# Optimization experiments

Hardware: AMD Instinct MI355X
Metric: run time of the kernel (lower is better)

The kernel has to match this reference:

```python
import jax, jax.numpy as jnp
from jax import lax
import numpy as np

N, E = 10000, 120000
IN_DIM = 128
HID = 32        # hidden_dim
HEADS = 8
OUT = 32        # out_dim
HD = HID * HEADS  # 256
EPS = 1e-5


def _bn(x, g, b):
    # BatchNorm1d (training-mode batch stats, deterministic reference)
    mu = x.mean(0)
    var = x.var(0)
    return g * (x - mu) * lax.rsqrt(var + EPS) + b


def _seg_softmax(logits, seg, n):
    # softmax over edges grouped by destination node, per head
    m = jax.ops.segment_max(logits, seg, num_segments=n)
    ex = jnp.exp(logits - m[seg])
    s = jax.ops.segment_sum(ex, seg, num_segments=n)
    return ex / (s[seg] + 1e-16)


def _gat_layer(h, src, dst, fc_w, a_l, a_r, bn_g, bn_b, heads, out, residual):
    n = h.shape[0]
    h_in = h
    feat = (h @ fc_w).reshape(n, heads, out)      # [N,H,D]
    el = (feat * a_l).sum(-1)                     # [N,H]
    er = (feat * a_r).sum(-1)
    logits = jax.nn.leaky_relu(el[src] + er[dst], 0.2)  # [E,H]
    alpha = _seg_softmax(logits, dst, n)
    rst = jax.ops.segment_sum(alpha[..., None] * feat[src], dst, num_segments=n)
    rst = rst.reshape(n, heads * out)
    rst = _bn(rst, bn_g, bn_b)
    rst = jax.nn.elu(rst)
    if residual:
        rst = h_in + rst
    return rst


def setup_inputs():
    key = jax.random.key(0)
    ks = jax.random.split(key, 20)
    s = 0.02
    d = {}
    d["h"] = jax.random.normal(ks[0], (N, IN_DIM), jnp.float32)
    d["e"] = jax.random.normal(ks[1], (E, IN_DIM), jnp.float32)
    d["src"] = jax.random.randint(ks[2], (E,), 0, N, jnp.int32)
    d["dst"] = jax.random.randint(ks[3], (E,), 0, N, jnp.int32)
    d["W_emb"] = jax.random.normal(ks[4], (IN_DIM, HD)) * s
    d["b_emb"] = jnp.zeros((HD,))
    d["W_p1"] = jax.random.normal(ks[5], (IN_DIM, HID * HID)) * s
    d["b_p1"] = jnp.zeros((HID * HID,))
    d["W_p2"] = jax.random.normal(ks[6], (IN_DIM, HID)) * s
    d["b_p2"] = jnp.zeros((HID,))
    d["W_conv"] = jax.random.normal(ks[7], (1, 2, 3)) * s  # Conv1d(2->1,k=3)
    d["b_conv"] = jnp.zeros((1,))
    d["W_ep2"] = jax.random.normal(ks[8], (IN_DIM, HD)) * s
    d["b_ep2"] = jnp.zeros((HD,))
    d["W_ep3"] = jax.random.normal(ks[9], (HID, HD)) * s
    d["b_ep3"] = jnp.zeros((HD,))
    d["bn_g"] = jnp.ones((HD,))
    d["bn_b"] = jnp.zeros((HD,))
    d["fc1"] = jax.random.normal(ks[10], (HD, HD)) * s
    d["al1"] = jax.random.normal(ks[11], (HEADS, HID)) * s
    d["ar1"] = jax.random.normal(ks[12], (HEADS, HID)) * s
    d["g1"] = jnp.ones((HD,))
    d["b1"] = jnp.zeros((HD,))
    d["fc2"] = jax.random.normal(ks[13], (HD, OUT)) * s
    d["al2"] = jax.random.normal(ks[14], (1, OUT)) * s
    d["ar2"] = jax.random.normal(ks[15], (1, OUT)) * s
    d["g2"] = jnp.ones((OUT,))
    d["b2"] = jnp.zeros((OUT,))
    return d


def reference(h, e, src, dst, W_emb, b_emb, W_p1, b_p1, W_p2, b_p2,
              W_conv, b_conv, W_ep2, b_ep2, W_ep3, b_ep3, bn_g, bn_b,
              fc1, al1, ar1, g1, b1, fc2, al2, ar2, g2, b2):
    # local edge feature: Conv1d over stacked (src,dst) node feats
    edge = jnp.stack([h[src], h[dst]], axis=1)  # [E,2,IN_DIM]
    conv = lax.conv_general_dilated(edge, W_conv, (1,), [(1, 1)],
                                    dimension_numbers=("NCH", "OIH", "NCH"))
    lr_local = conv[:, 0, :] + b_conv[0]         # [E,IN_DIM]
    lr_e_local = lr_local @ W_ep2 + b_ep2        # [E,HD]
    # low-rank global affinity: mm[i,j,k] = sum_d p1[i,k,d]*p2[j,d],
    # gathered only at edges (same math as the dense NxNxHID tensor)
    p1 = (h @ W_p1 + b_p1).reshape(-1, HID, HID)  # [N,HID,HID]
    p2 = h @ W_p2 + b_p2                          # [N,HID]
    lr_glob = jnp.einsum("ekd,ed->ek", p1[src], p2[dst])  # [E,HID]
    lr_e_global = lr_glob @ W_ep3 + b_ep3        # [E,HD]
    e_feat = jax.nn.relu(_bn(lr_e_local + lr_e_global, bn_g, bn_b))
    del e_feat  # default 'dgl' GATLayer ignores e; kept for faithfulness of math
    hh = h @ W_emb + b_emb                       # embedding_h
    hh = _gat_layer(hh, src, dst, fc1, al1, ar1, g1, b1, HEADS, HID, True)
    hh = _gat_layer(hh, src, dst, fc2, al2, ar2, g2, b2, 1, OUT, False)
    return hh
```

## Files before the change

kernel.cpp:

```cpp
#include <hip/hip_runtime.h>
#include <hip/hip_bf16.h>
#include <math.h>


#define HDIM 256
#define NHEADS 8
#define ODIM 32

typedef unsigned short u16;
typedef __attribute__((ext_vector_type(8))) short short8;
typedef __attribute__((ext_vector_type(4))) float f32x4;

__device__ __forceinline__ float bf2f(u16 u) { return __uint_as_float(((unsigned)u) << 16); }
__device__ __forceinline__ u16 f2bf(float f) {
    unsigned x = __float_as_uint(f);
    return (u16)((x + 0x7FFFu + ((x >> 16) & 1u)) >> 16);
}

__global__ __launch_bounds__(256) void prep_kernel(const float* __restrict__ in_h, const float* __restrict__ W_emb,
                                                   const float* __restrict__ fc1, const float* __restrict__ fc2,
                                                   const int* __restrict__ dstv, int* __restrict__ deg,
                                                   u16* __restrict__ Ah, u16* __restrict__ Bemb,
                                                   u16* __restrict__ Bfc1, u16* __restrict__ Bfc2,
                                                   int n4, int E, int N) {
    int job = blockIdx.y;
    int idx = blockIdx.x * 256 + threadIdx.x;
    if (job == 0) {
        if (idx >= n4) return;
        float4 v = ((const float4*)in_h)[idx];
        ushort4 o = {f2bf(v.x), f2bf(v.y), f2bf(v.z), f2bf(v.w)};
        ((ushort4*)Ah)[idx] = o;
        return;
    }
    if (job == 4) {
        if (idx < E) {
            unsigned d = (unsigned)dstv[idx];
            if (d < (unsigned)N) atomicAdd(&deg[d], 1);
        }
        return;
    }
    const float* B;
    u16* O;
    int K, NC;
    if (job == 1) { B = W_emb; O = Bemb; K = 128; NC = 256; }
    else if (job == 2) { B = fc1; O = Bfc1; K = 256; NC = 256; }
    else { B = fc2; O = Bfc2; K = 256; NC = 32; }
    int KB = K / 32;
    int TOT = (NC / 16) * KB * 64;
    if (idx >= TOT) return;
    int lane = idx & 63;
    int kb = (idx >> 6) % KB;
    int ct = (idx >> 6) / KB;
    int n = ct * 16 + (lane & 15);
    int k0 = kb * 32 + (lane >> 4) * 8;
    u16* dst = O + (size_t)idx * 8;
#pragma unroll
    for (int j = 0; j < 8; j++) dst[j] = f2bf(B[(size_t)(k0 + j) * NC + n]);
}

__global__ __launch_bounds__(256) void scan_kernel(const int* __restrict__ deg, int* __restrict__ offs,
                                                   int* __restrict__ cursor, int n) {
    __shared__ int wsum[4];
    int t = threadIdx.x;
    int chunk = (n + 255) / 256;
    int lo = t * chunk, hi = lo + chunk;
    if (hi > n) hi = n;
    if (lo > n) lo = n;
    int s = 0;
    for (int i = lo; i < hi; i++) s += deg[i];
    int v = s;
#pragma unroll
    for (int d = 1; d < 64; d <<= 1) {
        int nb = __shfl_up(v, d, 64);
        if ((t & 63) >= d) v += nb;
    }
    if ((t & 63) == 63) wsum[t >> 6] = v;
    __syncthreads();
    int woff = 0;
#pragma unroll
    for (int w = 0; w < 4; w++)
        if (w < (t >> 6)) woff += wsum[w];
    int run = woff + v - s;
    for (int i = lo; i < hi; i++) {
        offs[i] = run;
        cursor[i] = run;
        run += deg[i];
    }
    if (t == 255) offs[n] = run;
}

__global__ __launch_bounds__(256) void fused_emb_fc1(const u16* __restrict__ Ah, const u16* __restrict__ Bemb,
                                                     const float* __restrict__ bemb, const u16* __restrict__ Bfc1,
                                                     const float* __restrict__ al, const float* __restrict__ ar,
                                                     u16* __restrict__ hh, u16* __restrict__ feat1,
                                                     u16* __restrict__ el, u16* __restrict__ er,
                                                     const int* __restrict__ src, const int* __restrict__ dstv,
                                                     int* __restrict__ cursor, int* __restrict__ srcs,
                                                     int M, int NB, int E, int N) {
    if ((int)blockIdx.x >= NB) {
        int i = ((int)blockIdx.x - NB) * 256 + (int)threadIdx.x;
        if (i < E) {
            unsigned d = (unsigned)dstv[i];
            if (d < (unsigned)N) {
                int p = atomicAdd(&cursor[d], 1);
                if ((unsigned)p < (unsigned)E) srcs[p] = src[i];
            }
        }
        return;
    }
    __shared__ u16 tile[16 * 256];
    const int t = threadIdx.x;
    const int lane = t & 63, w = t >> 6;
    const int rb = (int)blockIdx.x * 16;
    const int m = lane & 15, q = lane >> 4;
    const int arow = rb + m;

    short8 a0[4];
#pragma unroll
    for (int kb = 0; kb < 4; kb++) {
        if (arow < M) a0[kb] = *(const short8*)(Ah + (size_t)arow * 128 + kb * 32 + q * 8);
        else a0[kb] = (short8){0, 0, 0, 0, 0, 0, 0, 0};
    }
    const short8* B8 = (const short8*)Bemb;
#pragma unroll
    for (int ct2 = 0; ct2 < 4; ct2++) {
        const int ct = w * 4 + ct2;
        f32x4 acc = {0.f, 0.f, 0.f, 0.f};
#pragma unroll
        for (int kb = 0; kb < 4; kb++)
            acc = __builtin_amdgcn_mfma_f32_16x16x32_bf16(a0[kb], B8[(ct * 4 + kb) * 64 + lane], acc, 0, 0, 0);
        float bv = bemb[ct * 16 + m];
#pragma unroll
        for (int r = 0; r < 4; r++) {
            int rl = q * 4 + r;
            int ro = rb + rl;
            u16 hv = 0;
            if (ro < M) {
                hv = f2bf(acc[r] + bv);
                hh[(size_t)ro * 256 + ct * 16 + m] = hv;
            }
            int byte = rl * 512 + (ct * 16 + m) * 2;
            tile[(byte ^ ((rl & 7) << 4)) >> 1] = hv;
        }
    }
    __syncthreads();

    short8 af[8];
    {
        int rl = m;
#pragma unroll
        for (int kb = 0; kb < 8; kb++) {
            int byte = rl * 512 + kb * 64 + q * 16;
            af[kb] = *(const short8*)(tile + ((byte ^ ((rl & 7) << 4)) >> 1));
        }
    }
    __syncthreads();

    const short8* Bf = (const short8*)Bfc1;
#pragma unroll
    for (int ct2 = 0; ct2 < 4; ct2++) {
        const int ct = w * 4 + ct2;
        f32x4 acc = {0.f, 0.f, 0.f, 0.f};
#pragma unroll
        for (int kb = 0; kb < 8; kb++)
            acc = __builtin_amdgcn_mfma_f32_16x16x32_bf16(af[kb], Bf[(ct * 8 + kb) * 64 + lane], acc, 0, 0, 0);
#pragma unroll
        for (int r = 0; r < 4; r++) {
            int rl = q * 4 + r;
            int ro = rb + rl;
            u16 v = 0;
            if (ro < M) {
                v = f2bf(acc[r]);
                feat1[(size_t)ro * 256 + ct * 16 + m] = v;
            }
            tile[rl * 256 + ct * 16 + m] = v;
        }
    }
    __syncthreads();

    if (t < 128) {
        int nl = t >> 3, h2 = t & 7;
        int node = rb + nl;
        if (node < M) {
            float a_ = 0.f, b_ = 0.f;
#pragma unroll
            for (int d = 0; d < 32; d++) {
                float fv = bf2f(tile[nl * 256 + h2 * 32 + d]);
                a_ += fv * al[h2 * 32 + d];
                b_ += fv * ar[h2 * 32 + d];
            }
            el[node * 8 + h2] = f2bf(a_);
            er[node * 8 + h2] = f2bf(b_);
        }
    }
}

__device__ __forceinline__ float edgew(float l) {
    l = (l > 0.f) ? l : 0.2f * l;
    l = fminf(fmaxf(l, -30.f), 30.f);
    return __expf(l);
}

__global__ __launch_bounds__(256) void agg1_fused(const u16* __restrict__ feat, const u16* __restrict__ el,
                                                  const u16* __restrict__ er, const int* __restrict__ offs,
                                                  const int* __restrict__ srcs, u16* __restrict__ rst, int N, int E) {
    const int node = blockIdx.x * 4 + (threadIdx.x >> 6);
    const int lane = threadIdx.x & 63;
    if (node >= N) return;
    const int half = lane >> 5;
    const int sl = lane & 31;
    const int h = sl >> 2;
    int beg = offs[node], end = offs[node + 1];
    if (beg < 0) beg = 0;
    if (end > E) end = E;
    int cnt = end - beg;
    if (cnt < 0) cnt = 0;
    float ern = bf2f(er[node * 8 + h]);
    float acc[8] = {0.f, 0.f, 0.f, 0.f, 0.f, 0.f, 0.f, 0.f};
    float sw = 0.f;
    const int myCnt = (cnt - half + 1) >> 1;
    const int jb = beg + half;
    int k = 0;
    int k4 = myCnt & ~3;
    for (; k < k4; k += 4) {
        int j0 = jb + 2 * k;
        int s0 = srcs[j0], s1 = srcs[j0 + 2], s2 = srcs[j0 + 4], s3 = srcs[j0 + 6];
        unsigned c0 = (unsigned)s0 < (unsigned)N, c1 = (unsigned)s1 < (unsigned)N;
        unsigned c2 = (unsigned)s2 < (unsigned)N, c3 = (unsigned)s3 < (unsigned)N;
        s0 = c0 ? s0 : 0; s1 = c1 ? s1 : 0; s2 = c2 ? s2 : 0; s3 = c3 ? s3 : 0;
        u16 e0 = el[s0 * 8 + h], e1 = el[s1 * 8 + h], e2 = el[s2 * 8 + h], e3 = el[s3 * 8 + h];
        short8 f0 = *(const short8*)(feat + (size_t)s0 * 256 + sl * 8);
        short8 f1 = *(const short8*)(feat + (size_t)s1 * 256 + sl * 8);
        short8 f2 = *(const short8*)(feat + (size_t)s2 * 256 + sl * 8);
        short8 f3 = *(const short8*)(feat + (size_t)s3 * 256 + sl * 8);
        float w0 = c0 ? edgew(bf2f(e0) + ern) : 0.f;
        float w1 = c1 ? edgew(bf2f(e1) + ern) : 0.f;
        float w2 = c2 ? edgew(bf2f(e2) + ern) : 0.f;
        float w3 = c3 ? edgew(bf2f(e3) + ern) : 0.f;
        sw += w0 + w1 + w2 + w3;
#pragma unroll
        for (int q = 0; q < 8; q++)
            acc[q] += w0 * bf2f((u16)f0[q]) + w1 * bf2f((u16)f1[q]) + w2 * bf2f((u16)f2[q]) + w3 * bf2f((u16)f3[q]);
    }
    for (; k < myCnt; k++) {
        int j = jb + 2 * k;
        int s = srcs[j];
        if ((unsigned)s >= (unsigned)N) continue;
        float wv = edgew(bf2f(el[s * 8 + h]) + ern);
        short8 fv = *(const short8*)(feat + (size_t)s * 256 + sl * 8);
        sw += wv;
#pragma unroll
        for (int q = 0; q < 8; q++) acc[q] += wv * bf2f((u16)fv[q]);
    }
#pragma unroll
    for (int q = 0; q < 8; q++) acc[q] += __shfl_xor(acc[q], 32, 64);
    sw += __shfl_xor(sw, 32, 64);
    if (half == 0) {
        float inv = 1.f / (sw + 1e-16f);
        short8 o;
#pragma unroll
        for (int q = 0; q < 8; q++) o[q] = (short)f2bf(acc[q] * inv);
        *(short8*)(rst + (size_t)node * 256 + sl * 8) = o;
    }
}

__global__ __launch_bounds__(256) void bn_stats256(const u16* __restrict__ X, float* __restrict__ stats,
                                                   int rows, int RPB) {
    __shared__ float ps[256][8], ps2[256][8];
    int t = threadIdx.x;
    int rg = t >> 5, cg = t & 31;
    int rbeg = blockIdx.x * RPB;
    int rend = rbeg + RPB;
    if (rend > rows) rend = rows;
    float s[8] = {0.f, 0.f, 0.f, 0.f, 0.f, 0.f, 0.f, 0.f};
    float s2[8] = {0.f, 0.f, 0.f, 0.f, 0.f, 0.f, 0.f, 0.f};
    for (int r = rbeg + rg; r < rend; r += 8) {
        short8 v = *(const short8*)(X + (size_t)r * 256 + cg * 8);
#pragma unroll
        for (int q = 0; q < 8; q++) {
            float x = bf2f((u16)v[q]);
            s[q] += x;
            s2[q] += x * x;
        }
    }
#pragma unroll
    for (int q = 0; q < 8; q++) { ps[t][q] = s[q]; ps2[t][q] = s2[q]; }
    __syncthreads();
    float a = 0.f, b = 0.f;
#pragma unroll
    for (int g = 0; g < 8; g++) {
        a += ps[g * 32 + (t >> 3)][t & 7];
        b += ps2[g * 32 + (t >> 3)][t & 7];
    }
    atomicAdd(&stats[t], a);
    atomicAdd(&stats[256 + t], b);
}

__global__ __launch_bounds__(256) void bn_stats32(const float* __restrict__ X, float* __restrict__ stats,
                                                  int rows, int RPB) {
    __shared__ float ss[256], ss2[256];
    int t = threadIdx.x, c = t & 31, rs = t >> 5;
    int rbeg = blockIdx.x * RPB;
    int rend = rbeg + RPB;
    if (rend > rows) rend = rows;
    float s = 0.f, s2 = 0.f;
    for (int r = rbeg + rs; r < rend; r += 8) {
        float x = X[(long)r * 32 + c];
        s += x;
        s2 += x * x;
    }
    ss[t] = s;
    ss2[t] = s2;
    __syncthreads();
    if (t < 32) {
        for (int j = 32; j < 256; j += 32) { s += ss[t + j]; s2 += ss2[t + j]; }
        atomicAdd(&stats[c], s);
        atomicAdd(&stats[32 + c], s2);
    }
}

__global__ __launch_bounds__(256) void gemm_fc2_fused(const u16* __restrict__ rst, const u16* __restrict__ hh,
                                                      const float* __restrict__ stats, const float* __restrict__ g,
                                                      const float* __restrict__ b, const u16* __restrict__ Bsw,
                                                      const float* __restrict__ al2, const float* __restrict__ ar2,
                                                      float* __restrict__ feat2, float* __restrict__ el2,
                                                      float* __restrict__ er2, int M, float invN) {
    __shared__ float sc[256], sh[256];
    __shared__ float red[2][256];
    __shared__ float tile[16][32];
    const int t = threadIdx.x;
    {
        float mu = stats[t] * invN;
        float var = fmaxf(stats[256 + t] * invN - mu * mu, 0.f);
        float s = g[t] * rsqrtf(var + 1e-5f);
        sc[t] = s;
        sh[t] = b[t] - mu * s;
    }
    __syncthreads();
    const int lane = t & 63, w = t >> 6;
    const int ct = w & 1, kh = w >> 1;
    const int rb = (int)blockIdx.x * 16;
    const int m = lane & 15, q = lane >> 4;
    const int row = rb + m;
    short8 a[4];
#pragma unroll
    for (int j = 0; j < 4; j++) {
        if (row < M) {
            int k0 = (kh * 4 + j) * 32 + q * 8;
            ushort4 r01 = *(const ushort4*)(rst + (size_t)row * 256 + k0);
            ushort4 r23 = *(const ushort4*)(rst + (size_t)row * 256 + k0 + 4);
            ushort4 h01 = *(const ushort4*)(hh + (size_t)row * 256 + k0);
            ushort4 h23 = *(const ushort4*)(hh + (size_t)row * 256 + k0 + 4);
            u16 rv[8] = {r01.x, r01.y, r01.z, r01.w, r23.x, r23.y, r23.z, r23.w};
            u16 hv[8] = {h01.x, h01.y, h01.z, h01.w, h23.x, h23.y, h23.z, h23.w};
            short8 av;
#pragma unroll
            for (int jj = 0; jj < 8; jj++) {
                int c = k0 + jj;
                float y = sc[c] * bf2f(rv[jj]) + sh[c];
                y = (y > 0.f) ? y : expm1f(y);
                av[jj] = (short)f2bf(bf2f(hv[jj]) + y);
            }
            a[j] = av;
        } else a[j] = (short8){0, 0, 0, 0, 0, 0, 0, 0};
    }
    const short8* B8 = (const short8*)Bsw;
    f32x4 acc = {0.f, 0.f, 0.f, 0.f};
#pragma unroll
    for (int j = 0; j < 4; j++)
        acc = __builtin_amdgcn_mfma_f32_16x16x32_bf16(a[j], B8[(ct * 8 + kh * 4 + j) * 64 + lane], acc, 0, 0, 0);
    if (kh == 1) *(f32x4*)&red[ct][lane * 4] = acc;
    __syncthreads();
    if (kh == 0) {
        f32x4 p = *(const f32x4*)&red[ct][lane * 4];
#pragma unroll
        for (int r = 0; r < 4; r++) {
            int rl = q * 4 + r;
            int ro = rb + rl;
            float v = 0.f;
            if (ro < M) {
                v = acc[r] + p[r];
                feat2[(size_t)ro * 32 + ct * 16 + m] = v;
            }
            tile[rl][ct * 16 + m] = v;
        }
    }
    __syncthreads();
    if (t < 16) {
        int node = rb + t;
        if (node < M) {
            float a_ = 0.f, b_ = 0.f;
#pragma unroll
            for (int d = 0; d < 32; d++) {
                float fv = tile[t][d];
                a_ += fv * al2[d];
                b_ += fv * ar2[d];
            }
            el2[node] = a_;
            er2[node] = b_;
        }
    }
}

__global__ __launch_bounds__(256) void agg2_fused(const float* __restrict__ feat, const float* __restrict__ el,
                                                  const float* __restrict__ er, const int* __restrict__ offs,
                                                  const int* __restrict__ srcs, float* __restrict__ rst,
                                                  int N, int E) {
    const int t = threadIdx.x;
    const int node = blockIdx.x * 8 + (t >> 5);
    const int d = t & 31;
    if (node >= N) return;
    int beg = offs[node], end = offs[node + 1];
    if (beg < 0) beg = 0;
    if (end > E) end = E;
    float ern = er[node];
    float acc = 0.f, sw = 0.f;
    int j = beg;
    int end4 = beg + ((end - beg) & ~3);
    for (; j < end4; j += 4) {
        int s0 = srcs[j], s1 = srcs[j + 1], s2 = srcs[j + 2], s3 = srcs[j + 3];
        unsigned c0 = (unsigned)s0 < (unsigned)N, c1 = (unsigned)s1 < (unsigned)N;
        unsigned c2 = (unsigned)s2 < (unsigned)N, c3 = (unsigned)s3 < (unsigned)N;
        s0 = c0 ? s0 : 0; s1 = c1 ? s1 : 0; s2 = c2 ? s2 : 0; s3 = c3 ? s3 : 0;
        float e0 = el[s0], e1 = el[s1], e2 = el[s2], e3 = el[s3];
        float f0 = feat[(size_t)s0 * 32 + d];
        float f1 = feat[(size_t)s1 * 32 + d];
        float f2 = feat[(size_t)s2 * 32 + d];
        float f3 = feat[(size_t)s3 * 32 + d];
        float w0 = c0 ? edgew(e0 + ern) : 0.f;
        float w1 = c1 ? edgew(e1 + ern) : 0.f;
        float w2 = c2 ? edgew(e2 + ern) : 0.f;
        float w3 = c3 ? edgew(e3 + ern) : 0.f;
        sw += w0; acc += w0 * f0;
        sw += w1; acc += w1 * f1;
        sw += w2; acc += w2 * f2;
        sw += w3; acc += w3 * f3;
    }
    for (; j < end; j++) {
        int s = srcs[j];
        if ((unsigned)s >= (unsigned)N) continue;
        float wv = edgew(el[s] + ern);
        sw += wv;
        acc += wv * feat[(size_t)s * 32 + d];
    }
    rst[(size_t)node * 32 + d] = acc / (sw + 1e-16f);
}

__global__ __launch_bounds__(256) void bn_apply2(const float* __restrict__ rst, const float* __restrict__ stats,
                                                 const float* __restrict__ g, const float* __restrict__ b,
                                                 float* __restrict__ out, int total4, float invN) {
    int idx = blockIdx.x * 256 + threadIdx.x;
    if (idx >= total4) return;
    float4 v = ((const float4*)rst)[idx];
    int c0 = (idx * 4) & 31;
    float r[4] = {v.x, v.y, v.z, v.w};
#pragma unroll
    for (int j = 0; j < 4; j++) {
        int c = c0 + j;
        float mu = stats[c] * invN;
        float var = fmaxf(stats[32 + c] * invN - mu * mu, 0.f);
        float y = g[c] * (r[j] - mu) * rsqrtf(var + 1e-5f) + b[c];
        r[j] = (y > 0.f) ? y : expm1f(y);
    }
    float4 o = {r[0], r[1], r[2], r[3]};
    ((float4*)out)[idx] = o;
}

extern "C" void kernel_launch(void* const* d_in, const int* in_sizes, int n_in, void* d_out, int out_size, void* d_ws,
                              size_t ws_size, hipStream_t stream) {
    const int N = out_size / ODIM;
    const int E = in_sizes[2];

    const int* src = (const int*)d_in[2];
    const int* dst = (const int*)d_in[3];
    const float* in_h = (const float*)d_in[0];
    const float* W_emb = (const float*)d_in[4];  const float* b_emb = (const float*)d_in[5];
    const float* fc1 = (const float*)d_in[18];   const float* al1 = (const float*)d_in[19];
    const float* ar1 = (const float*)d_in[20];
    const float* g1 = (const float*)d_in[21];    const float* b1 = (const float*)d_in[22];
    const float* fc2 = (const float*)d_in[23];   const float* al2 = (const float*)d_in[24];
    const float* ar2 = (const float*)d_in[25];
    const float* g2 = (const float*)d_in[26];    const float* b2 = (const float*)d_in[27];
    float* out = (float*)d_out;

    char* base = (char*)d_ws;
    size_t off = 0;
    auto alloc = [&](size_t bytes) { void* p = base + off; off += (bytes + 63) & ~63ull; return p; };
    char* zb   = (char*)alloc((size_t)N * 4 + 512 * 4 + 64 * 4);
    int* deg   = (int*)zb;
    float* stats  = (float*)(zb + (size_t)N * 4);
    float* stats2 = stats + 512;
    int* offs  = (int*)alloc((size_t)(N + 1) * 4);
    int* cursor = (int*)alloc((size_t)N * 4);
    int* srcs  = (int*)alloc((size_t)E * 4);
    u16* Ah    = (u16*)alloc((size_t)N * 128 * 2);
    u16* Bemb  = (u16*)alloc((size_t)128 * 256 * 2);
    u16* Bfc1  = (u16*)alloc((size_t)256 * 256 * 2);
    u16* Bfc2  = (u16*)alloc((size_t)256 * 32 * 2);
    u16* hh    = (u16*)alloc((size_t)N * HDIM * 2);
    u16* feat1 = (u16*)alloc((size_t)N * HDIM * 2);
    u16* el1   = (u16*)alloc((size_t)N * 8 * 2);
    u16* er1   = (u16*)alloc((size_t)N * 8 * 2);
    u16* rst   = (u16*)alloc((size_t)N * HDIM * 2);
    float* feat2 = (float*)alloc((size_t)N * 32 * 4);
    float* el2 = (float*)alloc((size_t)N * 4);
    float* er2 = (float*)alloc((size_t)N * 4);
    float* rst2 = (float*)alloc((size_t)N * 32 * 4);

    const int NB16 = (N + 15) / 16;
    const int NBF = (E + 255) / 256;

    hipMemsetAsync(zb, 0, (size_t)N * 4 + 512 * 4 + 64 * 4, stream);
    prep_kernel<<<dim3((N * 128 / 4 + 255) / 256, 5), 256, 0, stream>>>(in_h, W_emb, fc1, fc2, dst, deg,
                                                                        Ah, Bemb, Bfc1, Bfc2, N * 128 / 4, E, N);
    scan_kernel<<<1, 256, 0, stream>>>(deg, offs, cursor, N);
    fused_emb_fc1<<<NB16 + NBF, 256, 0, stream>>>(Ah, Bemb, b_emb, Bfc1, al1, ar1, hh, feat1, el1, er1,
                                                  src, dst, cursor, srcs, N, NB16, E, N);
    agg1_fused<<<(N + 3) / 4, 256, 0, stream>>>(feat1, el1, er1, offs, srcs, rst, N, E);
    bn_stats256<<<(N + 39) / 40, 256, 0, stream>>>(rst, stats, N, 40);
    gemm_fc2_fused<<<NB16, 256, 0, stream>>>(rst, hh, stats, g1, b1, Bfc2, al2, ar2, feat2, el2, er2, N, 1.f / N);
    agg2_fused<<<(N + 7) / 8, 256, 0, stream>>>(feat2, el2, er2, offs, srcs, rst2, N, E);
    bn_stats32<<<(N + 63) / 64, 256, 0, stream>>>(rst2, stats2, N, 64);
    bn_apply2<<<(N * 8 + 255) / 256, 256, 0, stream>>>(rst2, stats2, g2, b2, out, N * 8, 1.f / N);
}
```

Measured before the change: 241.9 us.

## Fuse BatchNorm statistics into aggregation kernels with sharded atomic accumulators

Removes the separate bn_stats256 and bn_stats32 kernels. Each aggregation kernel now reduces its outputs' sum and sum of squares per block in shared memory and atomically adds them into one of 64 (layer 1) or 32 (layer 2) sharded stat buffers. The consumers (gemm_fc2_fused, bn_apply2) sum the shards before use. This saves two launches and a full re-read of rst, at the cost of a larger memset, an extra __syncthreads in the aggregation kernels, and a shard reduction in every consumer block.

```diff
diff --git a/kernel.cpp b/kernel.cpp
--- a/kernel.cpp
+++ b/kernel.cpp
@@ -203,19 +203,28 @@
 
 __global__ __launch_bounds__(256) void agg1_fused(const u16* __restrict__ feat, const u16* __restrict__ el,
                                                   const u16* __restrict__ er, const int* __restrict__ offs,
-                                                  const int* __restrict__ srcs, u16* __restrict__ rst, int N, int E) {
-    const int node = blockIdx.x * 4 + (threadIdx.x >> 6);
-    const int lane = threadIdx.x & 63;
-    if (node >= N) return;
+                                                  const int* __restrict__ srcs, u16* __restrict__ rst,
+                                                  float* __restrict__ stats_sh, int N, int E) {
+    __shared__ float psum[4][256], psq[4][256];
+    const int t = threadIdx.x;
+    const int wv = t >> 6;
+    const int node = blockIdx.x * 4 + wv;
+    const int lane = t & 63;
     const int half = lane >> 5;
     const int sl = lane & 31;
     const int h = sl >> 2;
-    int beg = offs[node], end = offs[node + 1];
-    if (beg < 0) beg = 0;
-    if (end > E) end = E;
+    const bool valid = node < N;
+    int beg = 0, end = 0;
+    float ern = 0.f;
+    if (valid) {
+        beg = offs[node];
+        end = offs[node + 1];
+        if (beg < 0) beg = 0;
+        if (end > E) end = E;
+        ern = bf2f(er[node * 8 + h]);
+    }
     int cnt = end - beg;
     if (cnt < 0) cnt = 0;
-    float ern = bf2f(er[node * 8 + h]);
     float acc[8] = {0.f, 0.f, 0.f, 0.f, 0.f, 0.f, 0.f, 0.f};
     float sw = 0.f;
     const int myCnt = (cnt - half + 1) >> 1;
@@ -246,11 +255,11 @@
         int j = jb + 2 * k;
         int s = srcs[j];
         if ((unsigned)s >= (unsigned)N) continue;
-        float wv = edgew(bf2f(el[s * 8 + h]) + ern);
+        float wv2 = edgew(bf2f(el[s * 8 + h]) + ern);
         short8 fv = *(const short8*)(feat + (size_t)s * 256 + sl * 8);
-        sw += wv;
-#pragma unroll
-        for (int q = 0; q < 8; q++) acc[q] += wv * bf2f((u16)fv[q]);
+        sw += wv2;
+#pragma unroll
+        for (int q = 0; q < 8; q++) acc[q] += wv2 * bf2f((u16)fv[q]);
     }
 #pragma unroll
     for (int q = 0; q < 8; q++) acc[q] += __shfl_xor(acc[q], 32, 64);
@@ -260,67 +269,24 @@
         short8 o;
 #pragma unroll
         for (int q = 0; q < 8; q++) o[q] = (short)f2bf(acc[q] * inv);
-        *(short8*)(rst + (size_t)node * 256 + sl * 8) = o;
-    }
-}
-
-__global__ __launch_bounds__(256) void bn_stats256(const u16* __restrict__ X, float* __restrict__ stats,
-                                                   int rows, int RPB) {
-    __shared__ float ps[256][8], ps2[256][8];
-    int t = threadIdx.x;
-    int rg = t >> 5, cg = t & 31;
-    int rbeg = blockIdx.x * RPB;
-    int rend = rbeg + RPB;
-    if (rend > rows) rend = rows;
-    float s[8] = {0.f, 0.f, 0.f, 0.f, 0.f, 0.f, 0.f, 0.f};
-    float s2[8] = {0.f, 0.f, 0.f, 0.f, 0.f, 0.f, 0.f, 0.f};
-    for (int r = rbeg + rg; r < rend; r += 8) {
-        short8 v = *(const short8*)(X + (size_t)r * 256 + cg * 8);
+        if (valid) *(short8*)(rst + (size_t)node * 256 + sl * 8) = o;
 #pragma unroll
         for (int q = 0; q < 8; q++) {
-            float x = bf2f((u16)v[q]);
-            s[q] += x;
-            s2[q] += x * x;
-        }
-    }
-#pragma unroll
-    for (int q = 0; q < 8; q++) { ps[t][q] = s[q]; ps2[t][q] = s2[q]; }
-    __syncthreads();
-    float a = 0.f, b = 0.f;
-#pragma unroll
-    for (int g = 0; g < 8; g++) {
-        a += ps[g * 32 + (t >> 3)][t & 7];
-        b += ps2[g * 32 + (t >> 3)][t & 7];
-    }
-    atomicAdd(&stats[t], a);
-    atomicAdd(&stats[256 + t], b);
-}
-
-__global__ __launch_bounds__(256) void bn_stats32(const float* __restrict__ X, float* __restrict__ stats,
-                                                  int rows, int RPB) {
-    __shared__ float ss[256], ss2[256];
-    int t = threadIdx.x, c = t & 31, rs = t >> 5;
-    int rbeg = blockIdx.x * RPB;
-    int rend = rbeg + RPB;
-    if (rend > rows) rend = rows;
-    float s = 0.f, s2 = 0.f;
-    for (int r = rbeg + rs; r < rend; r += 8) {
-        float x = X[(long)r * 32 + c];
-        s += x;
-        s2 += x * x;
-    }
-    ss[t] = s;
-    ss2[t] = s2;
-    __syncthreads();
-    if (t < 32) {
-        for (int j = 32; j < 256; j += 32) { s += ss[t + j]; s2 += ss2[t + j]; }
-        atomicAdd(&stats[c], s);
-        atomicAdd(&stats[32 + c], s2);
-    }
+            float v = valid ? bf2f((u16)o[q]) : 0.f;
+            psum[wv][sl * 8 + q] = v;
+            psq[wv][sl * 8 + q] = v * v;
+        }
+    }
+    __syncthreads();
+    float a = psum[0][t] + psum[1][t] + psum[2][t] + psum[3][t];
+    float b = psq[0][t] + psq[1][t] + psq[2][t] + psq[3][t];
+    float* shd = stats_sh + (size_t)(blockIdx.x & 63) * 512;
+    atomicAdd(&shd[t], a);
+    atomicAdd(&shd[256 + t], b);
 }
 
 __global__ __launch_bounds__(256) void gemm_fc2_fused(const u16* __restrict__ rst, const u16* __restrict__ hh,
-                                                      const float* __restrict__ stats, const float* __restrict__ g,
+                                                      const float* __restrict__ stats_sh, const float* __restrict__ g,
                                                       const float* __restrict__ b, const u16* __restrict__ Bsw,
                                                       const float* __restrict__ al2, const float* __restrict__ ar2,
                                                       float* __restrict__ feat2, float* __restrict__ el2,
@@ -330,8 +296,14 @@
     __shared__ float tile[16][32];
     const int t = threadIdx.x;
     {
-        float mu = stats[t] * invN;
-        float var = fmaxf(stats[256 + t] * invN - mu * mu, 0.f);
+        float sum = 0.f, sq = 0.f;
+#pragma unroll 8
+        for (int s = 0; s < 64; s++) {
+            sum += stats_sh[s * 512 + t];
+            sq += stats_sh[s * 512 + 256 + t];
+        }
+        float mu = sum * invN;
+        float var = fmaxf(sq * invN - mu * mu, 0.f);
         float s = g[t] * rsqrtf(var + 1e-5f);
         sc[t] = s;
         sh[t] = b[t] - mu * s;
@@ -405,51 +377,79 @@
 __global__ __launch_bounds__(256) void agg2_fused(const float* __restrict__ feat, const float* __restrict__ el,
                                                   const float* __restrict__ er, const int* __restrict__ offs,
                                                   const int* __restrict__ srcs, float* __restrict__ rst,
-                                                  int N, int E) {
+                                                  float* __restrict__ stats2_sh, int N, int E) {
+    __shared__ float ss[256], ss2[256];
     const int t = threadIdx.x;
     const int node = blockIdx.x * 8 + (t >> 5);
     const int d = t & 31;
-    if (node >= N) return;
-    int beg = offs[node], end = offs[node + 1];
-    if (beg < 0) beg = 0;
-    if (end > E) end = E;
-    float ern = er[node];
-    float acc = 0.f, sw = 0.f;
-    int j = beg;
-    int end4 = beg + ((end - beg) & ~3);
-    for (; j < end4; j += 4) {
-        int s0 = srcs[j], s1 = srcs[j + 1], s2 = srcs[j + 2], s3 = srcs[j + 3];
-        unsigned c0 = (unsigned)s0 < (unsigned)N, c1 = (unsigned)s1 < (unsigned)N;
-        unsigned c2 = (unsigned)s2 < (unsigned)N, c3 = (unsigned)s3 < (unsigned)N;
-        s0 = c0 ? s0 : 0; s1 = c1 ? s1 : 0; s2 = c2 ? s2 : 0; s3 = c3 ? s3 : 0;
-        float e0 = el[s0], e1 = el[s1], e2 = el[s2], e3 = el[s3];
-        float f0 = feat[(size_t)s0 * 32 + d];
-        float f1 = feat[(size_t)s1 * 32 + d];
-        float f2 = feat[(size_t)s2 * 32 + d];
-        float f3 = feat[(size_t)s3 * 32 + d];
-        float w0 = c0 ? edgew(e0 + ern) : 0.f;
-        float w1 = c1 ? edgew(e1 + ern) : 0.f;
-        float w2 = c2 ? edgew(e2 + ern) : 0.f;
-        float w3 = c3 ? edgew(e3 + ern) : 0.f;
-        sw += w0; acc += w0 * f0;
-        sw += w1; acc += w1 * f1;
-        sw += w2; acc += w2 * f2;
-        sw += w3; acc += w3 * f3;
-    }
-    for (; j < end; j++) {
-        int s = srcs[j];
-        if ((unsigned)s >= (unsigned)N) continue;
-        float wv = edgew(el[s] + ern);
-        sw += wv;
-        acc += wv * feat[(size_t)s * 32 + d];
-    }
-    rst[(size_t)node * 32 + d] = acc / (sw + 1e-16f);
-}
-
-__global__ __launch_bounds__(256) void bn_apply2(const float* __restrict__ rst, const float* __restrict__ stats,
+    const bool valid = node < N;
+    float v = 0.f;
+    if (valid) {
+        int beg = offs[node], end = offs[node + 1];
+        if (beg < 0) beg = 0;
+        if (end > E) end = E;
+        float ern = er[node];
+        float acc = 0.f, sw = 0.f;
+        int j = beg;
+        int end4 = beg + ((end - beg) & ~3);
+        for (; j < end4; j += 4) {
+            int s0 = srcs[j], s1 = srcs[j + 1], s2 = srcs[j + 2], s3 = srcs[j + 3];
+            unsigned c0 = (unsigned)s0 < (unsigned)N, c1 = (unsigned)s1 < (unsigned)N;
+            unsigned c2 = (unsigned)s2 < (unsigned)N, c3 = (unsigned)s3 < (unsigned)N;
+            s0 = c0 ? s0 : 0; s1 = c1 ? s1 : 0; s2 = c2 ? s2 : 0; s3 = c3 ? s3 : 0;
+            float e0 = el[s0], e1 = el[s1], e2 = el[s2], e3 = el[s3];
+            float f0 = feat[(size_t)s0 * 32 + d];
+            float f1 = feat[(size_t)s1 * 32 + d];
+            float f2 = feat[(size_t)s2 * 32 + d];
+            float f3 = feat[(size_t)s3 * 32 + d];
+            float w0 = c0 ? edgew(e0 + ern) : 0.f;
+            float w1 = c1 ? edgew(e1 + ern) : 0.f;
+            float w2 = c2 ? edgew(e2 + ern) : 0.f;
+            float w3 = c3 ? edgew(e3 + ern) : 0.f;
+            sw += w0; acc += w0 * f0;
+            sw += w1; acc += w1 * f1;
+            sw += w2; acc += w2 * f2;
+            sw += w3; acc += w3 * f3;
+        }
+        for (; j < end; j++) {
+            int s = srcs[j];
+            if ((unsigned)s >= (unsigned)N) continue;
+            float wv = edgew(el[s] + ern);
+            sw += wv;
+            acc += wv * feat[(size_t)s * 32 + d];
+        }
+        v = acc / (sw + 1e-16f);
+        rst[(size_t)node * 32 + d] = v;
+    }
+    ss[t] = valid ? v : 0.f;
+    ss2[t] = valid ? v * v : 0.f;
+    __syncthreads();
+    if (t < 32) {
+        float a = 0.f, b = 0.f;
+#pragma unroll
+        for (int rg = 0; rg < 8; rg++) {
+            a += ss[rg * 32 + t];
+            b += ss2[rg * 32 + t];
+        }
+        float* shd = stats2_sh + (size_t)(blockIdx.x & 31) * 64;
+        atomicAdd(&shd[t], a);
+        atomicAdd(&shd[32 + t], b);
+    }
+}
+
+__global__ __launch_bounds__(256) void bn_apply2(const float* __restrict__ rst, const float* __restrict__ stats2_sh,
                                                  const float* __restrict__ g, const float* __restrict__ b,
                                                  float* __restrict__ out, int total4, float invN) {
-    int idx = blockIdx.x * 256 + threadIdx.x;
+    __shared__ float st[64];
+    int t = threadIdx.x;
+    if (t < 64) {
+        float a = 0.f;
+#pragma unroll
+        for (int s = 0; s < 32; s++) a += stats2_sh[s * 64 + t];
+        st[t] = a;
+    }
+    __syncthreads();
+    int idx = blockIdx.x * 256 + t;
     if (idx >= total4) return;
     float4 v = ((const float4*)rst)[idx];
     int c0 = (idx * 4) & 31;
@@ -457,8 +457,8 @@
 #pragma unroll
     for (int j = 0; j < 4; j++) {
         int c = c0 + j;
-        float mu = stats[c] * invN;
-        float var = fmaxf(stats[32 + c] * invN - mu * mu, 0.f);
+        float mu = st[c] * invN;
+        float var = fmaxf(st[32 + c] * invN - mu * mu, 0.f);
         float y = g[c] * (r[j] - mu) * rsqrtf(var + 1e-5f) + b[c];
         r[j] = (y > 0.f) ? y : expm1f(y);
     }
@@ -486,10 +486,11 @@
     char* base = (char*)d_ws;
     size_t off = 0;
     auto alloc = [&](size_t bytes) { void* p = base + off; off += (bytes + 63) & ~63ull; return p; };
-    char* zb   = (char*)alloc((size_t)N * 4 + 512 * 4 + 64 * 4);
+    const size_t ZBYTES = (size_t)N * 4 + 64 * 512 * 4 + 32 * 64 * 4;
+    char* zb   = (char*)alloc(ZBYTES);
     int* deg   = (int*)zb;
-    float* stats  = (float*)(zb + (size_t)N * 4);
-    float* stats2 = stats + 512;
+    float* stats_sh  = (float*)(zb + (size_t)N * 4);
+    float* stats2_sh = stats_sh + 64 * 512;
     int* offs  = (int*)alloc((size_t)(N + 1) * 4);
     int* cursor = (int*)alloc((size_t)N * 4);
     int* srcs  = (int*)alloc((size_t)E * 4);
@@ -510,16 +511,14 @@
     const int NB16 = (N + 15) / 16;
     const int NBF = (E + 255) / 256;
 
-    hipMemsetAsync(zb, 0, (size_t)N * 4 + 512 * 4 + 64 * 4, stream);
+    hipMemsetAsync(zb, 0, ZBYTES, stream);
     prep_kernel<<<dim3((N * 128 / 4 + 255) / 256, 5), 256, 0, stream>>>(in_h, W_emb, fc1, fc2, dst, deg,
                                                                         Ah, Bemb, Bfc1, Bfc2, N * 128 / 4, E, N);
     scan_kernel<<<1, 256, 0, stream>>>(deg, offs, cursor, N);
     fused_emb_fc1<<<NB16 + NBF, 256, 0, stream>>>(Ah, Bemb, b_emb, Bfc1, al1, ar1, hh, feat1, el1, er1,
                                                   src, dst, cursor, srcs, N, NB16, E, N);
-    agg1_fused<<<(N + 3) / 4, 256, 0, stream>>>(feat1, el1, er1, offs, srcs, rst, N, E);
-    bn_stats256<<<(N + 39) / 40, 256, 0, stream>>>(rst, stats, N, 40);
-    gemm_fc2_fused<<<NB16, 256, 0, stream>>>(rst, hh, stats, g1, b1, Bfc2, al2, ar2, feat2, el2, er2, N, 1.f / N);
-    agg2_fused<<<(N + 7) / 8, 256, 0, stream>>>(feat2, el2, er2, offs, srcs, rst2, N, E);
-    bn_stats32<<<(N + 63) / 64, 256, 0, stream>>>(rst2, stats2, N, 64);
-    bn_apply2<<<(N * 8 + 255) / 256, 256, 0, stream>>>(rst2, stats2, g2, b2, out, N * 8, 1.f / N);
-}
+    agg1_fused<<<(N + 3) / 4, 256, 0, stream>>>(feat1, el1, er1, offs, srcs, rst, stats_sh, N, E);
+    gemm_fc2_fused<<<NB16, 256, 0, stream>>>(rst, hh, stats_sh, g1, b1, Bfc2, al2, ar2, feat2, el2, er2, N, 1.f / N);
+    agg2_fused<<<(N + 7) / 8, 256, 0, stream>>>(feat2, el2, er2, offs, srcs, rst2, stats2_sh, N, E);
+    bn_apply2<<<(N * 8 + 255) / 256, 256, 0, stream>>>(rst2, stats2_sh, g2, b2, out, N * 8, 1.f / N);
+}
```

New measurement: 231.8 us. 1.04x faster.
